# Optimization experiments

Measured on AMD Instinct MI355X. Metric: run time of the kernel, lower is better.

Reference implementation:

```python
import jax, jax.numpy as jnp
import numpy as np

LN_EPS = 1e-6


def setup_inputs() -> dict:
    key = jax.random.key(0)
    ks = jax.random.split(key, 8)
    B, L, D = 8, 4096, 1024
    s = 1.0 / np.sqrt(D)
    inputs = jax.random.normal(ks[0], (B, L, D), dtype=jnp.float32)
    # PositionwiseFeedForward params (d_ff == d_model here)
    w1 = jax.random.normal(ks[1], (D, D), dtype=jnp.float32) * s
    b1 = jnp.zeros((D,), dtype=jnp.float32)
    w2 = jax.random.normal(ks[2], (D, D), dtype=jnp.float32) * s
    b2 = jnp.zeros((D,), dtype=jnp.float32)
    ln_g = jnp.ones((D,), dtype=jnp.float32)
    ln_b = jnp.zeros((D,), dtype=jnp.float32)
    # gating layer: Linear(2D, 2D)
    wg = jax.random.normal(ks[3], (2 * D, 2 * D), dtype=jnp.float32) * (1.0 / np.sqrt(2 * D))
    bg = jnp.zeros((2 * D,), dtype=jnp.float32)
    return {"inputs": inputs, "w1": w1, "b1": b1, "w2": w2, "b2": b2,
            "ln_g": ln_g, "ln_b": ln_b, "wg": wg, "bg": bg}


def _layer_norm(x, g, b):
    mu = jnp.mean(x, axis=-1, keepdims=True)
    var = jnp.mean(jnp.square(x - mu), axis=-1, keepdims=True)
    return (x - mu) * jax.lax.rsqrt(var + LN_EPS) * g + b


def reference(inputs, w1, b1, w2, b2, ln_g, ln_b, wg, bg):
    B, L, D = inputs.shape
    # Cumulative average: identical math to tril(ones)/arange mask @ inputs,
    # computed in O(L) via prefix sum instead of an O(L^2) matmul.
    denom = jnp.arange(1, L + 1, dtype=inputs.dtype)[:, None]  # [L,1]
    avg = jnp.cumsum(inputs, axis=1) / denom                    # [B,L,D]
    # PositionwiseFeedForward (eval mode, dropout=0): LN -> relu(Linear) -> Linear -> +residual
    h = _layer_norm(avg, ln_g, ln_b)
    inter = jax.nn.relu(jnp.einsum('bld,df->blf', h, w1) + b1)
    avg_out = jnp.einsum('blf,fd->bld', inter, w2) + b2 + avg
    # Gating: Linear on concat(inputs, avg_out), split, sigmoid gates
    concat = jnp.concatenate([inputs, avg_out], axis=-1)        # [B,L,2D]
    gates = jnp.einsum('ble,ef->blf', concat, wg) + bg          # [B,L,2D]
    input_gate, forget_gate = gates[..., :D], gates[..., D:]
    out = jax.nn.sigmoid(input_gate) * inputs + jax.nn.sigmoid(forget_gate) * avg_out
    return out
```

## Files before the change

### kernel.cpp

```cpp
#include <hip/hip_runtime.h>

typedef __bf16 bf16_t;
typedef bf16_t bf16x8 __attribute__((ext_vector_type(8)));
typedef bf16_t bf16x4 __attribute__((ext_vector_type(4)));
typedef float  f32x4  __attribute__((ext_vector_type(4)));

typedef const __attribute__((address_space(1))) void* gptr_t;
typedef __attribute__((address_space(3))) void* sptr_t;

#define BATCH 8
#define SEQL  4096
#define DIM   1024
#define MROWS 32768

__device__ __forceinline__ float sigmoidf_(float v) {
    return 1.0f / (1.0f + __expf(-v));
}

template <int PERM>
__global__ void transpose_cast(const float* __restrict__ W, bf16_t* __restrict__ WT,
                               int K, int N) {
    __shared__ float s[32][33];
    int tx = threadIdx.x, ty = threadIdx.y;
    int x = blockIdx.x * 32 + tx;
    int y = blockIdx.y * 32 + ty;
    s[ty][tx] = W[(size_t)y * N + x];
    __syncthreads();
    int n = blockIdx.x * 32 + ty;
    int k = blockIdx.y * 32 + tx;
    int nd = n;
    if (PERM) {
        if (n < 1024) nd = ((n >> 6) << 7) + (n & 63);
        else          nd = (((n - 1024) >> 6) << 7) + 64 + ((n - 1024) & 63);
    }
    WT[(size_t)nd * K + k] = (bf16_t)s[tx][ty];
}

__global__ void scan_chunks(const float* __restrict__ x, float* __restrict__ cs) {
    int tid = threadIdx.x;
    int b = blockIdx.x >> 6, c = blockIdx.x & 63;
    const f32x4* x4 = (const f32x4*)x;
    size_t base = ((size_t)b * SEQL + (size_t)c * 64) * 256 + tid;
    f32x4 s0 = {0.f, 0.f, 0.f, 0.f}, s1 = {0.f, 0.f, 0.f, 0.f};
#pragma unroll 8
    for (int j = 0; j < 64; j += 2) {
        s0 += x4[base + (size_t)j * 256];
        s1 += x4[base + (size_t)(j + 1) * 256];
    }
    ((f32x4*)cs)[((size_t)(b << 6) + c) * 256 + tid] = s0 + s1;
}

__global__ void scan_prefix(float* __restrict__ cs) {
    int t = blockIdx.x * 256 + threadIdx.x;
    int b = t >> 10, d = t & 1023;
    size_t base = (size_t)(b << 6) * 1024 + d;
    float v[64];
#pragma unroll
    for (int c = 0; c < 64; ++c) v[c] = cs[base + (size_t)c * 1024];
    float run = 0.f;
#pragma unroll
    for (int c = 0; c < 64; ++c) {
        float tv = v[c];
        cs[base + (size_t)c * 1024] = run;
        run += tv;
    }
}

__global__ __launch_bounds__(256) void scan_ln(
    const float* __restrict__ x, const float* __restrict__ cs,
    const float* __restrict__ g, const float* __restrict__ bb,
    float* __restrict__ avg, bf16_t* __restrict__ hb, bf16_t* __restrict__ xb) {
    int tid = threadIdx.x;
    int wave = tid >> 6, lane = tid & 63;
    int b = blockIdx.x >> 6, c = blockIdx.x & 63;
    __shared__ float red[8];
    const f32x4* x4 = (const f32x4*)x;
    f32x4* avg4 = (f32x4*)avg;
    bf16x4* hb4 = (bf16x4*)hb;
    bf16x4* xb4 = (bf16x4*)xb;
    f32x4 run = ((const f32x4*)cs)[((size_t)(b << 6) + c) * 256 + tid];
    f32x4 gv = ((const f32x4*)g)[tid];
    f32x4 bv = ((const f32x4*)bb)[tid];
    size_t row0 = (size_t)b * SEQL + (size_t)c * 64;
    f32x4 xv = x4[row0 * 256 + tid];
    for (int j = 0; j < 64; ++j) {
        size_t ridx = (row0 + j) * 256 + tid;
        f32x4 xnext = {0.f, 0.f, 0.f, 0.f};
        if (j < 63) xnext = x4[ridx + 256];
        run += xv;
        float inv = 1.0f / (float)(c * 64 + j + 1);
        f32x4 av = run * inv;
        avg4[ridx] = av;
        bf16x4 xo = { (bf16_t)xv[0], (bf16_t)xv[1], (bf16_t)xv[2], (bf16_t)xv[3] };
        xb4[ridx] = xo;
        float s  = av[0] + av[1] + av[2] + av[3];
        float sq = av[0]*av[0] + av[1]*av[1] + av[2]*av[2] + av[3]*av[3];
#pragma unroll
        for (int off = 32; off; off >>= 1) {
            s  += __shfl_xor(s, off);
            sq += __shfl_xor(sq, off);
        }
        if (lane == 0) { red[wave] = s; red[4 + wave] = sq; }
        __syncthreads();
        s  = red[0] + red[1] + red[2] + red[3];
        sq = red[4] + red[5] + red[6] + red[7];
        float mu  = s * (1.f / DIM);
        float var = sq * (1.f / DIM) - mu * mu;
        var = var < 0.f ? 0.f : var;
        float rs = 1.0f / sqrtf(var + 1e-6f);
        f32x4 hn = (av - mu) * rs * gv + bv;
        bf16x4 ho = { (bf16_t)hn[0], (bf16_t)hn[1], (bf16_t)hn[2], (bf16_t)hn[3] };
        hb4[ridx] = ho;
        __syncthreads();
        xv = xnext;
    }
}

template <int EPI>
__global__ __launch_bounds__(256) void gemm_bt(
    const bf16_t* __restrict__ A0, const bf16_t* __restrict__ A1, int kSplit,
    const bf16_t* __restrict__ Bt, int N, int K,
    const float* __restrict__ bias, const float* __restrict__ addsrc,
    const float* __restrict__ xsrc,
    float* __restrict__ outf, bf16_t* __restrict__ outb) {
    __shared__ char smem[128 * 64 * 2 * 2];
    bf16_t* As = (bf16_t*)smem;
    bf16_t* Bs = (bf16_t*)(smem + 128 * 64 * 2);
    const int tid = threadIdx.x;
    const int wave = tid >> 6, lane = tid & 63;
    const int nBlocks = N >> 7;
    const int m0 = (int)(blockIdx.x / nBlocks) << 7;
    const int n0 = (int)(blockIdx.x % nBlocks) << 7;
    const int wm = (wave & 1) << 6;
    const int wn = (wave >> 1) << 6;
    const int lrow16 = lane & 15;
    const int ksw0 = ((((lane >> 4) + 0) ^ (lane & 7)) << 3);
    const int ksw1 = ((((lane >> 4) + 4) ^ (lane & 7)) << 3);

    f32x4 acc[4][4] = {};

    for (int k0 = 0; k0 < K; k0 += 64) {
        __syncthreads();
        const bf16_t* Asrc;
        int ak0;
        if (k0 < kSplit) { Asrc = A0; ak0 = k0; }
        else             { Asrc = A1; ak0 = k0 - kSplit; }
#pragma unroll
        for (int rd = 0; rd < 4; ++rd) {
            int ci = tid + rd * 256;
            int row = ci >> 3, ch = ci & 7;
            int chs = ch ^ (row & 7);
            const bf16_t* gp = Asrc + (size_t)(m0 + row) * kSplit + ak0 + (chs << 3);
            bf16_t* sb = As + (size_t)(ci & ~63) * 8;
            __builtin_amdgcn_global_load_lds((gptr_t)gp, (sptr_t)sb, 16, 0, 0);
        }
#pragma unroll
        for (int rd = 0; rd < 4; ++rd) {
            int ci = tid + rd * 256;
            int row = ci >> 3, ch = ci & 7;
            int chs = ch ^ (row & 7);
            const bf16_t* gp = Bt + (size_t)(n0 + row) * K + k0 + (chs << 3);
            bf16_t* sb = Bs + (size_t)(ci & ~63) * 8;
            __builtin_amdgcn_global_load_lds((gptr_t)gp, (sptr_t)sb, 16, 0, 0);
        }
        __syncthreads();
#pragma unroll
        for (int kk = 0; kk < 2; ++kk) {
            const int ksw = kk ? ksw1 : ksw0;
            bf16x8 af[4], bfv[4];
#pragma unroll
            for (int mi = 0; mi < 4; ++mi)
                af[mi] = *(const bf16x8*)&As[(wm + mi * 16 + lrow16) * 64 + ksw];
#pragma unroll
            for (int ni = 0; ni < 4; ++ni)
                bfv[ni] = *(const bf16x8*)&Bs[(wn + ni * 16 + lrow16) * 64 + ksw];
#pragma unroll
            for (int mi = 0; mi < 4; ++mi)
#pragma unroll
                for (int ni = 0; ni < 4; ++ni)
                    acc[mi][ni] = __builtin_amdgcn_mfma_f32_16x16x32_bf16(
                        af[mi], bfv[ni], acc[mi][ni], 0, 0, 0);
        }
    }

    const int erow = (lane >> 4) << 2;

    if (EPI == 4) {
        __syncthreads();
        float* xch = (float*)smem;
        const int T = n0 >> 7;
        const int mloc = (wm >> 6) * 4096;
        if (wave >= 2) {
#pragma unroll
            for (int mi = 0; mi < 4; ++mi) {
#pragma unroll
                for (int ni = 0; ni < 4; ++ni) {
                    int dc = ni * 16 + lrow16;
                    float bcol = bias[1024 + T * 64 + dc];
                    int d = T * 64 + dc;
#pragma unroll
                    for (int r = 0; r < 4; ++r) {
                        int row = m0 + wm + mi * 16 + erow + r;
                        float v = acc[mi][ni][r] + bcol;
                        float part = sigmoidf_(v) * addsrc[(size_t)row * 1024 + d];
                        xch[mloc + (mi * 16 + erow + r) * 64 + dc] = part;
                    }
                }
            }
        }
        __syncthreads();
        if (wave < 2) {
#pragma unroll
            for (int mi = 0; mi < 4; ++mi) {
#pragma unroll
                for (int ni = 0; ni < 4; ++ni) {
                    int dc = ni * 16 + lrow16;
                    float bcol = bias[T * 64 + dc];
                    int d = T * 64 + dc;
#pragma unroll
                    for (int r = 0; r < 4; ++r) {
                        int row = m0 + wm + mi * 16 + erow + r;
                        float v = acc[mi][ni][r] + bcol;
                        float tot = sigmoidf_(v) * xsrc[(size_t)row * 1024 + d]
                                  + xch[mloc + (mi * 16 + erow + r) * 64 + dc];
                        outf[(size_t)row * 1024 + d] = tot;
                    }
                }
            }
        }
        return;
    }

#pragma unroll
    for (int mi = 0; mi < 4; ++mi) {
#pragma unroll
        for (int ni = 0; ni < 4; ++ni) {
            int col = n0 + wn + ni * 16 + lrow16;
            float bcol = bias[col];
#pragma unroll
            for (int r = 0; r < 4; ++r) {
                int row = m0 + wm + mi * 16 + erow + r;
                size_t idx = (size_t)row * N + col;
                float v = acc[mi][ni][r];
                if (EPI == 1) {
                    v += bcol;
                    v = v > 0.f ? v : 0.f;
                    outb[idx] = (bf16_t)v;
                } else {
                    v += bcol + addsrc[idx];
                    outf[idx] = v;
                    outb[idx] = (bf16_t)v;
                }
            }
        }
    }
}

extern "C" void kernel_launch(void* const* d_in, const int* in_sizes, int n_in,
                              void* d_out, int out_size, void* d_ws, size_t ws_size,
                              hipStream_t stream) {
    const float* inp  = (const float*)d_in[0];
    const float* w1   = (const float*)d_in[1];
    const float* b1   = (const float*)d_in[2];
    const float* w2   = (const float*)d_in[3];
    const float* b2   = (const float*)d_in[4];
    const float* ln_g = (const float*)d_in[5];
    const float* ln_b = (const float*)d_in[6];
    const float* wg   = (const float*)d_in[7];
    const float* bg   = (const float*)d_in[8];
    float* out = (float*)d_out;

    char* w = (char*)d_ws;
    float*  avg    = (float*)w;   w += (size_t)MROWS * DIM * 4;
    float*  avgout = (float*)w;   w += (size_t)MROWS * DIM * 4;
    bf16_t* xb     = (bf16_t*)w;  w += (size_t)MROWS * DIM * 2;
    bf16_t* hb     = (bf16_t*)w;  w += (size_t)MROWS * DIM * 2;
    bf16_t* interb = (bf16_t*)w;  w += (size_t)MROWS * DIM * 2;
    bf16_t* w1t    = (bf16_t*)w;  w += (size_t)DIM * DIM * 2;
    bf16_t* w2t    = (bf16_t*)w;  w += (size_t)DIM * DIM * 2;
    bf16_t* wgt    = (bf16_t*)w;  w += (size_t)2 * DIM * 2 * DIM * 2;
    float*  csum   = (float*)w;   w += (size_t)BATCH * 64 * DIM * 4;
    bf16_t* aob    = hb;

    transpose_cast<0><<<dim3(32, 32), dim3(32, 32), 0, stream>>>(w1, w1t, DIM, DIM);
    transpose_cast<0><<<dim3(32, 32), dim3(32, 32), 0, stream>>>(w2, w2t, DIM, DIM);
    transpose_cast<1><<<dim3(64, 64), dim3(32, 32), 0, stream>>>(wg, wgt, 2 * DIM, 2 * DIM);

    scan_chunks<<<BATCH * 64, 256, 0, stream>>>(inp, csum);
    scan_prefix<<<32, 256, 0, stream>>>(csum);
    scan_ln<<<BATCH * 64, 256, 0, stream>>>(inp, csum, ln_g, ln_b, avg, hb, xb);

    gemm_bt<1><<<(MROWS / 128) * (DIM / 128), 256, 0, stream>>>(
        hb, hb, DIM, w1t, DIM, DIM, b1, nullptr, nullptr, nullptr, interb);

    gemm_bt<2><<<(MROWS / 128) * (DIM / 128), 256, 0, stream>>>(
        interb, interb, DIM, w2t, DIM, DIM, b2, avg, nullptr, avgout, aob);

    gemm_bt<4><<<(MROWS / 128) * (2 * DIM / 128), 256, 0, stream>>>(
        xb, aob, DIM, wgt, 2 * DIM, 2 * DIM, bg, avgout, inp, out, nullptr);
}
```

Baseline: 1.075 ms.

## Enlarge GEMM tiles to 256x256 with double-buffered LDS pipeline and XCD-aware block remap

```diff
diff --git a/kernel.cpp b/kernel.cpp
--- a/kernel.cpp
+++ b/kernel.cpp
@@ -117,37 +117,43 @@
 }
 
 template <int EPI>
-__global__ __launch_bounds__(256) void gemm_bt(
+__global__ __launch_bounds__(512, 2) void gemm_bt(
     const bf16_t* __restrict__ A0, const bf16_t* __restrict__ A1, int kSplit,
     const bf16_t* __restrict__ Bt, int N, int K,
     const float* __restrict__ bias, const float* __restrict__ addsrc,
     const float* __restrict__ xsrc,
     float* __restrict__ outf, bf16_t* __restrict__ outb) {
-    __shared__ char smem[128 * 64 * 2 * 2];
-    bf16_t* As = (bf16_t*)smem;
-    bf16_t* Bs = (bf16_t*)(smem + 128 * 64 * 2);
+    __shared__ char smem[131072];
     const int tid = threadIdx.x;
     const int wave = tid >> 6, lane = tid & 63;
-    const int nBlocks = N >> 7;
-    const int m0 = (int)(blockIdx.x / nBlocks) << 7;
-    const int n0 = (int)(blockIdx.x % nBlocks) << 7;
-    const int wm = (wave & 1) << 6;
-    const int wn = (wave >> 1) << 6;
+
+    const int nwg = gridDim.x;
+    const int q8 = nwg >> 3;
+    const int lid = (blockIdx.x & 7) * q8 + ((int)blockIdx.x >> 3);
+    const int nBlocks = N >> 8;
+    const int m0 = (lid / nBlocks) << 8;
+    const int n0 = (lid % nBlocks) << 8;
+
+    const int wm = (wave >> 2) << 7;
+    const int wn = (wave & 3) << 6;
     const int lrow16 = lane & 15;
     const int ksw0 = ((((lane >> 4) + 0) ^ (lane & 7)) << 3);
     const int ksw1 = ((((lane >> 4) + 4) ^ (lane & 7)) << 3);
 
-    f32x4 acc[4][4] = {};
-
-    for (int k0 = 0; k0 < K; k0 += 64) {
-        __syncthreads();
+    f32x4 acc[8][4] = {};
+
+    const int nT = K >> 6;
+
+    auto STAGE = [&](int k0, int buf) {
         const bf16_t* Asrc;
         int ak0;
         if (k0 < kSplit) { Asrc = A0; ak0 = k0; }
         else             { Asrc = A1; ak0 = k0 - kSplit; }
+        bf16_t* As = (bf16_t*)(smem + buf * 65536);
+        bf16_t* Bs = As + 256 * 64;
 #pragma unroll
         for (int rd = 0; rd < 4; ++rd) {
-            int ci = tid + rd * 256;
+            int ci = tid + (rd << 9);
             int row = ci >> 3, ch = ci & 7;
             int chs = ch ^ (row & 7);
             const bf16_t* gp = Asrc + (size_t)(m0 + row) * kSplit + ak0 + (chs << 3);
@@ -156,30 +162,52 @@
         }
 #pragma unroll
         for (int rd = 0; rd < 4; ++rd) {
-            int ci = tid + rd * 256;
+            int ci = tid + (rd << 9);
             int row = ci >> 3, ch = ci & 7;
             int chs = ch ^ (row & 7);
             const bf16_t* gp = Bt + (size_t)(n0 + row) * K + k0 + (chs << 3);
             bf16_t* sb = Bs + (size_t)(ci & ~63) * 8;
             __builtin_amdgcn_global_load_lds((gptr_t)gp, (sptr_t)sb, 16, 0, 0);
         }
-        __syncthreads();
-#pragma unroll
-        for (int kk = 0; kk < 2; ++kk) {
+    };
+
+    STAGE(0, 0);
+
+    for (int t = 0; t < nT; ++t) {
+        const int p = t & 1;
+        __builtin_amdgcn_s_barrier();
+        if (t + 1 < nT) {
+            STAGE((t + 1) << 6, p ^ 1);
+            asm volatile("s_waitcnt vmcnt(8)" ::: "memory");
+        } else {
+            asm volatile("s_waitcnt vmcnt(0)" ::: "memory");
+        }
+        __builtin_amdgcn_s_barrier();
+        __builtin_amdgcn_sched_barrier(0);
+        const bf16_t* As = (const bf16_t*)(smem + p * 65536);
+        const bf16_t* Bs = As + 256 * 64;
+        bf16x8 bfv[4];
+#pragma unroll
+        for (int ph = 0; ph < 4; ++ph) {
+            const int kk = ph >> 1, mh = ph & 1;
             const int ksw = kk ? ksw1 : ksw0;
-            bf16x8 af[4], bfv[4];
+            if (mh == 0) {
+#pragma unroll
+                for (int ni = 0; ni < 4; ++ni)
+                    bfv[ni] = *(const bf16x8*)&Bs[(wn + ni * 16 + lrow16) * 64 + ksw];
+            }
+            bf16x8 af[4];
 #pragma unroll
             for (int mi = 0; mi < 4; ++mi)
-                af[mi] = *(const bf16x8*)&As[(wm + mi * 16 + lrow16) * 64 + ksw];
-#pragma unroll
-            for (int ni = 0; ni < 4; ++ni)
-                bfv[ni] = *(const bf16x8*)&Bs[(wn + ni * 16 + lrow16) * 64 + ksw];
+                af[mi] = *(const bf16x8*)&As[(wm + (mh * 4 + mi) * 16 + lrow16) * 64 + ksw];
+            __builtin_amdgcn_s_setprio(1);
 #pragma unroll
             for (int mi = 0; mi < 4; ++mi)
 #pragma unroll
                 for (int ni = 0; ni < 4; ++ni)
-                    acc[mi][ni] = __builtin_amdgcn_mfma_f32_16x16x32_bf16(
-                        af[mi], bfv[ni], acc[mi][ni], 0, 0, 0);
+                    acc[mh * 4 + mi][ni] = __builtin_amdgcn_mfma_f32_16x16x32_bf16(
+                        af[mi], bfv[ni], acc[mh * 4 + mi][ni], 0, 0, 0);
+            __builtin_amdgcn_s_setprio(0);
         }
     }
 
@@ -188,11 +216,11 @@
     if (EPI == 4) {
         __syncthreads();
         float* xch = (float*)smem;
-        const int T = n0 >> 7;
-        const int mloc = (wm >> 6) * 4096;
-        if (wave >= 2) {
-#pragma unroll
-            for (int mi = 0; mi < 4; ++mi) {
+        const int T = (n0 + wn) >> 7;
+        const int pairOff = ((((wave >> 2) << 1) | ((wave >> 1) & 1))) << 13;
+        if (wn & 64) {
+#pragma unroll
+            for (int mi = 0; mi < 8; ++mi) {
 #pragma unroll
                 for (int ni = 0; ni < 4; ++ni) {
                     int dc = ni * 16 + lrow16;
@@ -200,18 +228,20 @@
                     int d = T * 64 + dc;
 #pragma unroll
                     for (int r = 0; r < 4; ++r) {
-                        int row = m0 + wm + mi * 16 + erow + r;
+                        int rowW = mi * 16 + erow + r;
+                        int row = m0 + wm + rowW;
                         float v = acc[mi][ni][r] + bcol;
-                        float part = sigmoidf_(v) * addsrc[(size_t)row * 1024 + d];
-                        xch[mloc + (mi * 16 + erow + r) * 64 + dc] = part;
+                        int sw = ((rowW >> 2) & 1) << 4;
+                        xch[pairOff + rowW * 64 + (dc ^ sw)] =
+                            sigmoidf_(v) * addsrc[(size_t)row * 1024 + d];
                     }
                 }
             }
         }
         __syncthreads();
-        if (wave < 2) {
-#pragma unroll
-            for (int mi = 0; mi < 4; ++mi) {
+        if (!(wn & 64)) {
+#pragma unroll
+            for (int mi = 0; mi < 8; ++mi) {
 #pragma unroll
                 for (int ni = 0; ni < 4; ++ni) {
                     int dc = ni * 16 + lrow16;
@@ -219,10 +249,12 @@
                     int d = T * 64 + dc;
 #pragma unroll
                     for (int r = 0; r < 4; ++r) {
-                        int row = m0 + wm + mi * 16 + erow + r;
+                        int rowW = mi * 16 + erow + r;
+                        int row = m0 + wm + rowW;
                         float v = acc[mi][ni][r] + bcol;
+                        int sw = ((rowW >> 2) & 1) << 4;
                         float tot = sigmoidf_(v) * xsrc[(size_t)row * 1024 + d]
-                                  + xch[mloc + (mi * 16 + erow + r) * 64 + dc];
+                                  + xch[pairOff + rowW * 64 + (dc ^ sw)];
                         outf[(size_t)row * 1024 + d] = tot;
                     }
                 }
@@ -232,7 +264,7 @@
     }
 
 #pragma unroll
-    for (int mi = 0; mi < 4; ++mi) {
+    for (int mi = 0; mi < 8; ++mi) {
 #pragma unroll
         for (int ni = 0; ni < 4; ++ni) {
             int col = n0 + wn + ni * 16 + lrow16;
@@ -290,12 +322,12 @@
     scan_prefix<<<32, 256, 0, stream>>>(csum);
     scan_ln<<<BATCH * 64, 256, 0, stream>>>(inp, csum, ln_g, ln_b, avg, hb, xb);
 
-    gemm_bt<1><<<(MROWS / 128) * (DIM / 128), 256, 0, stream>>>(
+    gemm_bt<1><<<(MROWS / 256) * (DIM / 256), 512, 0, stream>>>(
         hb, hb, DIM, w1t, DIM, DIM, b1, nullptr, nullptr, nullptr, interb);
 
-    gemm_bt<2><<<(MROWS / 128) * (DIM / 128), 256, 0, stream>>>(
+    gemm_bt<2><<<(MROWS / 256) * (DIM / 256), 512, 0, stream>>>(
         interb, interb, DIM, w2t, DIM, DIM, b2, avg, nullptr, avgout, aob);
 
-    gemm_bt<4><<<(MROWS / 128) * (2 * DIM / 128), 256, 0, stream>>>(
+    gemm_bt<4><<<(MROWS / 256) * (2 * DIM / 256), 512, 0, stream>>>(
         xb, aob, DIM, wgt, 2 * DIM, 2 * DIM, bg, avgout, inp, out, nullptr);
 }
```

Measured after the change: 942.4 us. 12.3% less time.
